# Optimization experiments

Hardware: AMD Instinct MI355X
Metric: run time of the kernel (lower is better)

## Reference

```python
import jax, jax.numpy as jnp
import numpy as np

B, C, H, W = 4, 256, 64, 64
CP = C // 4  # embedding_channels, k=4 hardcoded
# branch index -> (key-stream i, query/value-stream j); streams: 0=t,1=b,2=m
IIDX = np.array([0, 0, 0, 1, 1, 1, 2, 2, 2])  # which stream feeds k
JIDX = np.array([0, 1, 2, 0, 1, 2, 0, 1, 2])  # which stream feeds q and v


def setup_inputs() -> dict:
    key = jax.random.key(0)
    ks = jax.random.split(key, 6)
    scale = 0.05
    return {
        "t": jax.random.normal(ks[0], (B, C, H, W), jnp.float32),
        "b": jax.random.normal(ks[1], (B, C, H, W), jnp.float32),
        "m": jax.random.normal(ks[2], (B, C, H, W), jnp.float32),
        "W_qkv": jax.random.normal(ks[3], (9, C, C), jnp.float32) * scale,
        "W_red": jax.random.normal(ks[4], (9, CP, C), jnp.float32) * scale,
        "W_rec": jax.random.normal(ks[5], (9, C, CP), jnp.float32) * scale,
    }


def _pool(x):
    # ChannelAttention: global avg pool + global max pool -> [B, C']
    return jnp.mean(x, axis=(2, 3)) + jnp.max(x, axis=(2, 3))


def _channel_attention(q, k, v, w_red, w_rec):
    # q,k,v: [B,C,H,W]; w_red: [C',C]; w_rec: [C,C']
    ori = q + k + v
    red = lambda x: jax.nn.relu(jnp.einsum("bchw,ec->behw", x, w_red))
    qr, kr, vr = red(q), red(k), red(v)
    f = _pool(kr)  # key   -> [B,C']
    g = _pool(qr)  # query -> [B,C']
    h = _pool(vr)  # value -> [B,C']
    # s = f^T g : [B,C',C']; softmax over dim=1 (rows), per torch nn.Softmax(dim=1)
    s = f[:, :, None] * g[:, None, :]
    beta = jax.nn.softmax(s, axis=1)
    vout = jnp.einsum("bi,bij->bj", h, beta)  # [B,C']
    # recovery 1x1 conv on [B,C',1,1]; bilinear upsample from 1x1 == broadcast
    o = jax.nn.sigmoid(jnp.einsum("be,ce->bc", vout, w_rec))  # [B,C]
    return o[:, :, None, None] * ori


def reference(t, b, m, W_qkv, W_red, W_rec):
    x = jnp.stack([t, b, m])  # [3,B,C,H,W]
    Wp = W_qkv.reshape(3, 3, C, C)  # [stream, (q,k,v), C_out, C_in]
    proj = jnp.einsum("sbchw,sjec->sjbehw", x, Wp)  # [3,3,B,C,H,W]
    Q, K, V = proj[:, 0], proj[:, 1], proj[:, 2]  # each [3,B,C,H,W]
    q9, k9, v9 = Q[JIDX], K[IIDX], V[JIDX]  # [9,B,C,H,W]
    outs = jax.vmap(_channel_attention)(q9, k9, v9, W_red, W_rec)
    return outs.sum(axis=0)
```

## Files before the change

kernel.cpp:

```cpp
#include <hip/hip_runtime.h>

#define Bn 4
#define Cn 256
#define HWn 4096
#define CPn 64
#define MP 640

typedef unsigned short u16;
typedef unsigned int u32;

using short8  = __attribute__((ext_vector_type(8))) short;
using floatx4 = __attribute__((ext_vector_type(4))) float;

static __device__ __forceinline__ u16 f2bf(float f) {
    union { float f; u32 u; } v; v.f = f;
    u32 r = (v.u + 0x7FFFu + ((v.u >> 16) & 1u)) >> 16;
    return (u16)r;
}

static __device__ __forceinline__ void gld16(const u16* g, u16* l) {
    __builtin_amdgcn_global_load_lds(
        (const __attribute__((address_space(1))) u32*)g,
        (__attribute__((address_space(3))) u32*)l, 16, 0, 0);
}


__global__ __launch_bounds__(256) void convert_transpose(
    const float* __restrict__ Tt, const float* __restrict__ Bt, const float* __restrict__ Mt,
    u16* __restrict__ xT)
{
    const int s  = blockIdx.z, b = blockIdx.y;
    const int ct = blockIdx.x & 3, hwt = blockIdx.x >> 2;
    const int c0 = ct * 64, hw0 = hwt * 64;
    const float* X = (s == 0 ? Tt : (s == 1 ? Bt : Mt)) + (size_t)b * Cn * HWn;

    __shared__ u16 T[64][72];
    const int t = threadIdx.x;
    const int cl = t >> 2, q = t & 3;

    const float* src = X + (size_t)(c0 + cl) * HWn + hw0 + q * 16;
    #pragma unroll
    for (int u = 0; u < 4; ++u) {
        const float4 v = *(const float4*)(src + u * 4);
        T[cl][q * 16 + u * 4 + 0] = f2bf(v.x);
        T[cl][q * 16 + u * 4 + 1] = f2bf(v.y);
        T[cl][q * 16 + u * 4 + 2] = f2bf(v.z);
        T[cl][q * 16 + u * 4 + 3] = f2bf(v.w);
    }
    __syncthreads();

    const int wl = t >> 2;
    u16* dst = xT + ((size_t)((s * Bn + b) * HWn) + hw0 + wl) * Cn + c0 + q * 16;
    #pragma unroll
    for (int u = 0; u < 2; ++u) {
        u32 w0 = (u32)T[q * 16 + u * 8 + 0][wl] | ((u32)T[q * 16 + u * 8 + 1][wl] << 16);
        u32 w1 = (u32)T[q * 16 + u * 8 + 2][wl] | ((u32)T[q * 16 + u * 8 + 3][wl] << 16);
        u32 w2 = (u32)T[q * 16 + u * 8 + 4][wl] | ((u32)T[q * 16 + u * 8 + 5][wl] << 16);
        u32 w3 = (u32)T[q * 16 + u * 8 + 6][wl] | ((u32)T[q * 16 + u * 8 + 7][wl] << 16);
        uint4 pk = {w0, w1, w2, w3};
        *(uint4*)(dst + u * 8) = pk;
    }
}

__global__ __launch_bounds__(256) void compose_red(
    const float* __restrict__ Wqkv, const float* __restrict__ Wred,
    u16* __restrict__ CWp)
{
    const int s  = blockIdx.z;
    const int tt = blockIdx.y / 3, m3 = blockIdx.y % 3;
    const int c0 = blockIdx.x * 64;
    const int idx = (tt == 1) ? (3 * s + m3) : (3 * m3 + s);

    const float* A = Wred + (size_t)idx * CPn * Cn;
    const float* Bm = Wqkv + (size_t)(3 * s + tt) * Cn * Cn;

    __shared__ float As[16][64];
    __shared__ float Bs[16][64];
    const int t = threadIdx.x;
    const int ty = t >> 4, tx = t & 15;
    float acc[4][4] = {};

    for (int k0 = 0; k0 < Cn; k0 += 16) {
        {
            const int r = t >> 2, eq = (t & 3) * 4;
            const float4 a = *(const float4*)(A + (size_t)r * Cn + k0 + eq);
            As[eq + 0][r] = a.x; As[eq + 1][r] = a.y; As[eq + 2][r] = a.z; As[eq + 3][r] = a.w;
        }
        {
            const int r = t >> 4, cq = (t & 15) * 4;
            *(float4*)(&Bs[r][cq]) = *(const float4*)(Bm + (size_t)(k0 + r) * Cn + c0 + cq);
        }
        __syncthreads();
        #pragma unroll
        for (int k = 0; k < 16; ++k) {
            const float4 a4 = *(const float4*)(&As[k][ty * 4]);
            const float4 b4 = *(const float4*)(&Bs[k][tx * 4]);
            const float a[4] = {a4.x, a4.y, a4.z, a4.w};
            const float bb[4] = {b4.x, b4.y, b4.z, b4.w};
            #pragma unroll
            for (int i = 0; i < 4; ++i)
                #pragma unroll
                for (int j = 0; j < 4; ++j)
                    acc[i][j] = fmaf(a[i], bb[j], acc[i][j]);
        }
        __syncthreads();
    }

    u16* out = CWp + (size_t)s * MP * Cn;
    #pragma unroll
    for (int i = 0; i < 4; ++i) {
        const int row = tt * 192 + m3 * 64 + ty * 4 + i;
        unsigned long long pk =
            (unsigned long long)f2bf(acc[i][0]) |
            ((unsigned long long)f2bf(acc[i][1]) << 16) |
            ((unsigned long long)f2bf(acc[i][2]) << 32) |
            ((unsigned long long)f2bf(acc[i][3]) << 48);
        *(unsigned long long*)(out + (size_t)row * Cn + c0 + tx * 4) = pk;
    }
}

__global__ __launch_bounds__(256, 2) void redpool_mfma(
    const u16* __restrict__ xT, const u16* __restrict__ CWp,
    float* __restrict__ pool_sum, u32* __restrict__ pool_max)
{
    const int s  = blockIdx.z;
    const int mt = blockIdx.x >> 6, nt = blockIdx.x & 63;
    const int m0 = mt * 128, n0 = nt * 256;

    const u16* Ap = CWp + (size_t)s * MP * Cn;
    const u16* Bp = xT + (size_t)s * Bn * HWn * Cn;

    __shared__ __align__(16) u16 As[16 * 512];
    __shared__ __align__(16) u16 Bs[32 * 512];

    const int t = threadIdx.x;
    const int w = t >> 6, lane = t & 63;
    const int l15 = lane & 15, q = lane >> 4;
    const int rb = (w >> 1) * 64, cb = (w & 1) * 128;

    floatx4 acc[4][8] = {};

    for (int k0 = 0; k0 < Cn; k0 += 64) {
        const u16* Asrc = Ap + (size_t)m0 * Cn + k0 + (size_t)l15 * Cn + q * 8;
        const u16* Bsrc = Bp + (size_t)n0 * Cn + k0 + (size_t)l15 * Cn + q * 8;
        #pragma unroll
        for (int pi = 0; pi < 4; ++pi) {
            const int p = w * 4 + pi;
            gld16(Asrc + (size_t)((p >> 1) * 16) * Cn + (p & 1) * 32, &As[p * 512]);
        }
        #pragma unroll
        for (int pi = 0; pi < 8; ++pi) {
            const int p = w * 8 + pi;
            gld16(Bsrc + (size_t)((p >> 1) * 16) * Cn + (p & 1) * 32, &Bs[p * 512]);
        }
        __syncthreads();
        #pragma unroll
        for (int kk = 0; kk < 2; ++kk) {
            short8 af[4], bf[8];
            #pragma unroll
            for (int i = 0; i < 4; ++i)
                af[i] = *(const short8*)&As[((((w >> 1) * 4 + i) << 1) + kk) * 512 + lane * 8];
            #pragma unroll
            for (int j = 0; j < 8; ++j)
                bf[j] = *(const short8*)&Bs[((((w & 1) * 8 + j) << 1) + kk) * 512 + lane * 8];
            #pragma unroll
            for (int i = 0; i < 4; ++i)
                #pragma unroll
                for (int j = 0; j < 8; ++j)
                    acc[i][j] = __builtin_amdgcn_mfma_f32_16x16x32_bf16(af[i], bf[j], acc[i][j], 0, 0, 0);
        }
        __syncthreads();
    }

    const int b = n0 >> 12;
    #pragma unroll
    for (int i = 0; i < 4; ++i) {
        #pragma unroll
        for (int r = 0; r < 4; ++r) {
            float rs = 0.f, rm = 0.f;
            #pragma unroll
            for (int j = 0; j < 8; ++j) {
                const float v = fmaxf(acc[i][j][r], 0.f);
                rs += v; rm = fmaxf(rm, v);
            }
            #pragma unroll
            for (int off = 1; off < 16; off <<= 1) {
                rs += __shfl_xor(rs, off);
                rm = fmaxf(rm, __shfl_xor(rm, off));
            }
            if (l15 == 0) {
                const int R = m0 + rb + i * 16 + q * 4 + r;
                if (R < 576) {
                    const int tt = R / 192, m3 = (R / 64) % 3, cp = R & 63;
                    const int idx = (tt == 1) ? (3 * s + m3) : (3 * m3 + s);
                    const int pidx = ((tt * 9 + idx) * Bn + b) * CPn + cp;
                    atomicAdd(&pool_sum[pidx], rs);
                    atomicMax(&pool_max[pidx], __float_as_uint(rm));
                }
            }
        }
    }
}

__global__ __launch_bounds__(256) void attn_small(
    const float* __restrict__ pool_sum, const u32* __restrict__ pool_max,
    const float* __restrict__ Wrec,
    float* __restrict__ coefA, float* __restrict__ coefK)
{
    const int idx = blockIdx.x / Bn;
    const int bb  = blockIdx.x % Bn;
    __shared__ float ff[CPn], gg[CPn], hh[CPn], vout[CPn];
    const int t = threadIdx.x;

    if (t < CPn) {
        int base;
        base = ((0 * 9 + idx) * Bn + bb) * CPn + t;
        gg[t] = pool_sum[base] * (1.0f / HWn) + __uint_as_float(pool_max[base]);
        base = ((1 * 9 + idx) * Bn + bb) * CPn + t;
        ff[t] = pool_sum[base] * (1.0f / HWn) + __uint_as_float(pool_max[base]);
        base = ((2 * 9 + idx) * Bn + bb) * CPn + t;
        hh[t] = pool_sum[base] * (1.0f / HWn) + __uint_as_float(pool_max[base]);
    }
    __syncthreads();

    if (t < CPn) {
        const float gj = gg[t];
        float mx = -1e30f;
        for (int i = 0; i < CPn; ++i) mx = fmaxf(mx, ff[i] * gj);
        float den = 0.f, num = 0.f;
        for (int i = 0; i < CPn; ++i) {
            const float e = expf(ff[i] * gj - mx);
            den += e;
            num += hh[i] * e;
        }
        vout[t] = num / den;
    }
    __syncthreads();

    {
        const float* wr = Wrec + ((size_t)idx * Cn + t) * CPn;
        float a = 0.f;
        for (int e = 0; e < CPn; ++e) a += vout[e] * wr[e];
        const float o = 1.0f / (1.0f + expf(-a));
        const int sj = idx % 3;
        const int si = idx / 3;
        atomicAdd(coefA + (sj * Bn + bb) * Cn + t, o);
        atomicAdd(coefK + (si * Bn + bb) * Cn + t, o);
    }
}

__global__ __launch_bounds__(256) void build_M(
    const float* __restrict__ Wqkv,
    const float* __restrict__ coefA, const float* __restrict__ coefK,
    u16* __restrict__ Mm)
{
    const int s = blockIdx.x >> 8, m = blockIdx.x & 255;
    const int b = blockIdx.y;
    const int t = threadIdx.x;
    const float cA = coefA[(s * Bn + b) * Cn + m];
    const float cK = coefK[(s * Bn + b) * Cn + m];
    const float wq = Wqkv[((size_t)(3 * s + 0) * Cn + m) * Cn + t];
    const float wk = Wqkv[((size_t)(3 * s + 1) * Cn + m) * Cn + t];
    const float wv = Wqkv[((size_t)(3 * s + 2) * Cn + m) * Cn + t];
    Mm[((size_t)(b * 256 + m)) * 768 + s * 256 + t] = f2bf(cA * (wq + wv) + cK * wk);
}

__global__ __launch_bounds__(256, 2) void final_mfma(
    const u16* __restrict__ xT, const u16* __restrict__ Mm,
    float* __restrict__ out)
{
    const int b  = blockIdx.y;
    const int mt = blockIdx.x >> 5, nt = blockIdx.x & 31;
    const int m0 = mt * 128, n0 = nt * 128;

    __shared__ __align__(16) u16 As[16 * 512];
    __shared__ __align__(16) u16 Bs[16 * 512];

    const int t = threadIdx.x;
    const int w = t >> 6, lane = t & 63;
    const int l15 = lane & 15, q = lane >> 4;
    const int rb = (w >> 1) * 64, cb = (w & 1) * 64;

    const u16* Apb = Mm + (size_t)(b * 256 + m0) * 768;

    floatx4 acc[4][4] = {};

    for (int k0 = 0; k0 < 768; k0 += 64) {
        const int s = k0 >> 8, c0 = k0 & 255;
        const u16* Asrc = Apb + k0 + (size_t)l15 * 768 + q * 8;
        const u16* Bsrc = xT + ((size_t)((s * Bn + b) * HWn) + n0 + l15) * Cn + c0 + q * 8;
        #pragma unroll
        for (int pi = 0; pi < 4; ++pi) {
            const int p = w * 4 + pi;
            gld16(Asrc + (size_t)((p >> 1) * 16) * 768 + (p & 1) * 32, &As[p * 512]);
            gld16(Bsrc + (size_t)((p >> 1) * 16) * Cn + (p & 1) * 32, &Bs[p * 512]);
        }
        __syncthreads();
        #pragma unroll
        for (int kk = 0; kk < 2; ++kk) {
            short8 af[4], bf[4];
            #pragma unroll
            for (int i = 0; i < 4; ++i)
                af[i] = *(const short8*)&As[((((w >> 1) * 4 + i) << 1) + kk) * 512 + lane * 8];
            #pragma unroll
            for (int j = 0; j < 4; ++j)
                bf[j] = *(const short8*)&Bs[((((w & 1) * 4 + j) << 1) + kk) * 512 + lane * 8];
            #pragma unroll
            for (int i = 0; i < 4; ++i)
                #pragma unroll
                for (int j = 0; j < 4; ++j)
                    acc[i][j] = __builtin_amdgcn_mfma_f32_16x16x32_bf16(af[i], bf[j], acc[i][j], 0, 0, 0);
        }
        __syncthreads();
    }

    #pragma unroll
    for (int i = 0; i < 4; ++i)
        #pragma unroll
        for (int j = 0; j < 4; ++j)
            #pragma unroll
            for (int r = 0; r < 4; ++r) {
                const int row = m0 + rb + i * 16 + q * 4 + r;
                const int col = n0 + cb + j * 16 + l15;
                out[((size_t)(b * 256) + row) * HWn + col] = acc[i][j][r];
            }
}

extern "C" void kernel_launch(void* const* d_in, const int* in_sizes, int n_in,
                              void* d_out, int out_size, void* d_ws, size_t ws_size,
                              hipStream_t stream)
{
    const float* Tt   = (const float*)d_in[0];
    const float* Bt   = (const float*)d_in[1];
    const float* Mt   = (const float*)d_in[2];
    const float* Wqkv = (const float*)d_in[3];
    const float* Wred = (const float*)d_in[4];
    const float* Wrec = (const float*)d_in[5];
    float* out = (float*)d_out;

    unsigned char* p = (unsigned char*)d_ws;
    u16* xT = (u16*)p;            p += (size_t)3 * Bn * HWn * Cn * 2;
    u16* Mm = (u16*)p;            p += (size_t)Bn * 256 * 768 * 2;
    unsigned char* zbase = p;
    u16* CWp = (u16*)p;           p += (size_t)3 * MP * Cn * 2;
    float* pool_sum = (float*)p;  p += (size_t)27 * Bn * CPn * 4;
    u32*   pool_max = (u32*)p;    p += (size_t)27 * Bn * CPn * 4;
    float* coefA = (float*)p;     p += (size_t)3 * Bn * Cn * 4;
    float* coefK = (float*)p;     p += (size_t)3 * Bn * Cn * 4;
    const size_t zbytes = (size_t)(p - zbase);

    hipMemsetAsync(zbase, 0, zbytes, stream);

    compose_red      <<<dim3(4, 9, 3),    256, 0, stream>>>(Wqkv, Wred, CWp);
    convert_transpose<<<dim3(256, Bn, 3), 256, 0, stream>>>(Tt, Bt, Mt, xT);
    redpool_mfma     <<<dim3(320, 1, 3),  256, 0, stream>>>(xT, CWp, pool_sum, pool_max);
    attn_small       <<<9 * Bn,           256, 0, stream>>>(pool_sum, pool_max, Wrec, coefA, coefK);
    build_M          <<<dim3(768, Bn),    256, 0, stream>>>(Wqkv, coefA, coefK, Mm);
    final_mfma       <<<dim3(64, Bn),     256, 0, stream>>>(xT, Mm, out);
}
```

Baseline: 188.4 us.

## Replace pool atomics with per-tile partials and shrink final GEMM tile

The reduction-pool kernel no longer does global atomicAdd/atomicMax per row. It combines the two column-halves in shared memory and writes one partial sum and max per (row, column tile), which attn_small then reduces over 16 tiles. The final GEMM tile narrows from 128 to 64 columns, doubling the grid to fill more compute units. Both kernels also drop the occupancy hint of 2 from launch_bounds. This removes atomic contention and the zeroing of the pool buffers, at the cost of an extra partial buffer, a small serial reduction, and more reloads of the A operand in the final GEMM.

```diff
diff --git a/kernel.cpp b/kernel.cpp
--- a/kernel.cpp
+++ b/kernel.cpp
@@ -119,9 +119,9 @@
     }
 }
 
-__global__ __launch_bounds__(256, 2) void redpool_mfma(
+__global__ __launch_bounds__(256) void redpool_mfma(
     const u16* __restrict__ xT, const u16* __restrict__ CWp,
-    float* __restrict__ pool_sum, u32* __restrict__ pool_max)
+    float* __restrict__ Psum, float* __restrict__ Pmax)
 {
     const int s  = blockIdx.z;
     const int mt = blockIdx.x >> 6, nt = blockIdx.x & 63;
@@ -132,11 +132,13 @@
 
     __shared__ __align__(16) u16 As[16 * 512];
     __shared__ __align__(16) u16 Bs[32 * 512];
+    __shared__ float Lsum[2][128];
+    __shared__ float Lmax[2][128];
 
     const int t = threadIdx.x;
     const int w = t >> 6, lane = t & 63;
     const int l15 = lane & 15, q = lane >> 4;
-    const int rb = (w >> 1) * 64, cb = (w & 1) * 128;
+    const int rb = (w >> 1) * 64;
 
     floatx4 acc[4][8] = {};
 
@@ -172,7 +174,7 @@
         __syncthreads();
     }
 
-    const int b = n0 >> 12;
+    const int wi = w & 1;
     #pragma unroll
     for (int i = 0; i < 4; ++i) {
         #pragma unroll
@@ -189,21 +191,22 @@
                 rm = fmaxf(rm, __shfl_xor(rm, off));
             }
             if (l15 == 0) {
-                const int R = m0 + rb + i * 16 + q * 4 + r;
-                if (R < 576) {
-                    const int tt = R / 192, m3 = (R / 64) % 3, cp = R & 63;
-                    const int idx = (tt == 1) ? (3 * s + m3) : (3 * m3 + s);
-                    const int pidx = ((tt * 9 + idx) * Bn + b) * CPn + cp;
-                    atomicAdd(&pool_sum[pidx], rs);
-                    atomicMax(&pool_max[pidx], __float_as_uint(rm));
-                }
-            }
-        }
+                const int lr = rb + 16 * i + q * 4 + r;
+                Lsum[wi][lr] = rs;
+                Lmax[wi][lr] = rm;
+            }
+        }
+    }
+    __syncthreads();
+    if (t < 128) {
+        const int R = m0 + t;
+        Psum[((size_t)s * MP + R) * 64 + nt] = Lsum[0][t] + Lsum[1][t];
+        Pmax[((size_t)s * MP + R) * 64 + nt] = fmaxf(Lmax[0][t], Lmax[1][t]);
     }
 }
 
 __global__ __launch_bounds__(256) void attn_small(
-    const float* __restrict__ pool_sum, const u32* __restrict__ pool_max,
+    const float* __restrict__ Psum, const float* __restrict__ Pmax,
     const float* __restrict__ Wrec,
     float* __restrict__ coefA, float* __restrict__ coefK)
 {
@@ -213,13 +216,24 @@
     const int t = threadIdx.x;
 
     if (t < CPn) {
-        int base;
-        base = ((0 * 9 + idx) * Bn + bb) * CPn + t;
-        gg[t] = pool_sum[base] * (1.0f / HWn) + __uint_as_float(pool_max[base]);
-        base = ((1 * 9 + idx) * Bn + bb) * CPn + t;
-        ff[t] = pool_sum[base] * (1.0f / HWn) + __uint_as_float(pool_max[base]);
-        base = ((2 * 9 + idx) * Bn + bb) * CPn + t;
-        hh[t] = pool_sum[base] * (1.0f / HWn) + __uint_as_float(pool_max[base]);
+        float v[3];
+        #pragma unroll
+        for (int tt = 0; tt < 3; ++tt) {
+            const int s_ = (tt == 1) ? idx / 3 : idx % 3;
+            const int m3 = (tt == 1) ? idx % 3 : idx / 3;
+            const int R  = tt * 192 + m3 * 64 + t;
+            const size_t base = ((size_t)s_ * MP + R) * 64 + bb * 16;
+            float sm = 0.f, mx = 0.f;
+            #pragma unroll
+            for (int u = 0; u < 16; ++u) {
+                sm += Psum[base + u];
+                mx = fmaxf(mx, Pmax[base + u]);
+            }
+            v[tt] = sm * (1.0f / HWn) + mx;
+        }
+        gg[t] = v[0];
+        ff[t] = v[1];
+        hh[t] = v[2];
     }
     __syncthreads();
 
@@ -265,25 +279,25 @@
     Mm[((size_t)(b * 256 + m)) * 768 + s * 256 + t] = f2bf(cA * (wq + wv) + cK * wk);
 }
 
-__global__ __launch_bounds__(256, 2) void final_mfma(
+__global__ __launch_bounds__(256) void final_mfma(
     const u16* __restrict__ xT, const u16* __restrict__ Mm,
     float* __restrict__ out)
 {
     const int b  = blockIdx.y;
-    const int mt = blockIdx.x >> 5, nt = blockIdx.x & 31;
-    const int m0 = mt * 128, n0 = nt * 128;
+    const int mt = blockIdx.x >> 6, nt = blockIdx.x & 63;
+    const int m0 = mt * 128, n0 = nt * 64;
 
     __shared__ __align__(16) u16 As[16 * 512];
-    __shared__ __align__(16) u16 Bs[16 * 512];
+    __shared__ __align__(16) u16 Bs[8 * 512];
 
     const int t = threadIdx.x;
     const int w = t >> 6, lane = t & 63;
     const int l15 = lane & 15, q = lane >> 4;
-    const int rb = (w >> 1) * 64, cb = (w & 1) * 64;
+    const int rb = (w >> 1) * 64, cb = (w & 1) * 32;
 
     const u16* Apb = Mm + (size_t)(b * 256 + m0) * 768;
 
-    floatx4 acc[4][4] = {};
+    floatx4 acc[4][2] = {};
 
     for (int k0 = 0; k0 < 768; k0 += 64) {
         const int s = k0 >> 8, c0 = k0 & 255;
@@ -293,22 +307,26 @@
         for (int pi = 0; pi < 4; ++pi) {
             const int p = w * 4 + pi;
             gld16(Asrc + (size_t)((p >> 1) * 16) * 768 + (p & 1) * 32, &As[p * 512]);
+        }
+        #pragma unroll
+        for (int pi = 0; pi < 2; ++pi) {
+            const int p = w * 2 + pi;
             gld16(Bsrc + (size_t)((p >> 1) * 16) * Cn + (p & 1) * 32, &Bs[p * 512]);
         }
         __syncthreads();
         #pragma unroll
         for (int kk = 0; kk < 2; ++kk) {
-            short8 af[4], bf[4];
+            short8 af[4], bf[2];
             #pragma unroll
             for (int i = 0; i < 4; ++i)
                 af[i] = *(const short8*)&As[((((w >> 1) * 4 + i) << 1) + kk) * 512 + lane * 8];
             #pragma unroll
-            for (int j = 0; j < 4; ++j)
-                bf[j] = *(const short8*)&Bs[((((w & 1) * 4 + j) << 1) + kk) * 512 + lane * 8];
+            for (int j = 0; j < 2; ++j)
+                bf[j] = *(const short8*)&Bs[((((w & 1) * 2 + j) << 1) + kk) * 512 + lane * 8];
             #pragma unroll
             for (int i = 0; i < 4; ++i)
                 #pragma unroll
-                for (int j = 0; j < 4; ++j)
+                for (int j = 0; j < 2; ++j)
                     acc[i][j] = __builtin_amdgcn_mfma_f32_16x16x32_bf16(af[i], bf[j], acc[i][j], 0, 0, 0);
         }
         __syncthreads();
@@ -317,7 +335,7 @@
     #pragma unroll
     for (int i = 0; i < 4; ++i)
         #pragma unroll
-        for (int j = 0; j < 4; ++j)
+        for (int j = 0; j < 2; ++j)
             #pragma unroll
             for (int r = 0; r < 4; ++r) {
                 const int row = m0 + rb + i * 16 + q * 4 + r;
@@ -341,10 +359,10 @@
     unsigned char* p = (unsigned char*)d_ws;
     u16* xT = (u16*)p;            p += (size_t)3 * Bn * HWn * Cn * 2;
     u16* Mm = (u16*)p;            p += (size_t)Bn * 256 * 768 * 2;
+    float* Psum = (float*)p;      p += (size_t)3 * MP * 64 * 4;
+    float* Pmax = (float*)p;      p += (size_t)3 * MP * 64 * 4;
     unsigned char* zbase = p;
     u16* CWp = (u16*)p;           p += (size_t)3 * MP * Cn * 2;
-    float* pool_sum = (float*)p;  p += (size_t)27 * Bn * CPn * 4;
-    u32*   pool_max = (u32*)p;    p += (size_t)27 * Bn * CPn * 4;
     float* coefA = (float*)p;     p += (size_t)3 * Bn * Cn * 4;
     float* coefK = (float*)p;     p += (size_t)3 * Bn * Cn * 4;
     const size_t zbytes = (size_t)(p - zbase);
@@ -353,8 +371,8 @@
 
     compose_red      <<<dim3(4, 9, 3),    256, 0, stream>>>(Wqkv, Wred, CWp);
     convert_transpose<<<dim3(256, Bn, 3), 256, 0, stream>>>(Tt, Bt, Mt, xT);
-    redpool_mfma     <<<dim3(320, 1, 3),  256, 0, stream>>>(xT, CWp, pool_sum, pool_max);
-    attn_small       <<<9 * Bn,           256, 0, stream>>>(pool_sum, pool_max, Wrec, coefA, coefK);
+    redpool_mfma     <<<dim3(320, 1, 3),  256, 0, stream>>>(xT, CWp, Psum, Pmax);
+    attn_small       <<<9 * Bn,           256, 0, stream>>>(Psum, Pmax, Wrec, coefA, coefK);
     build_M          <<<dim3(768, Bn),    256, 0, stream>>>(Wqkv, coefA, coefK, Mm);
-    final_mfma       <<<dim3(64, Bn),     256, 0, stream>>>(xT, Mm, out);
-}
+    final_mfma       <<<dim3(128, Bn),    256, 0, stream>>>(xT, Mm, out);
+}
```

Result: slower. 210.6 us (+11.8%).
